# Kernel tuning notes

Hardware: AMD Instinct MI355X
Metric: run time of the kernel (lower is better)

## Reference

```python
import jax, jax.numpy as jnp
import numpy as np

T, B, H, V, D = 128, 16, 8, 25, 64


def setup_inputs() -> dict:
    key = jax.random.key(0)
    k1, k2, k3 = jax.random.split(key, 3)
    q = jax.random.uniform(k1, (T, B, H, V, D), dtype=jnp.float32)
    kv = jax.random.uniform(k2, (T, B, H, V, D), dtype=jnp.float32)
    # decay factor in (0,1), per-head per-channel, as in the torch module
    decay = jax.random.uniform(k3, (1, 1, H, 1, D), dtype=jnp.float32)
    return {"q": q, "kv": kv, "decay": decay}


def reference(q, kv, decay):
    """Decay-based linear recurrent state-space scan (RetNet-style):
        S_t = decay * S_{t-1} + (1 - decay) * kv_t
        out_t = q_t * S_t
    q, kv: (T, B, H, V, D); decay: (1, 1, H, 1, D).
    """
    d = decay[0, 0]          # (H, 1, D), broadcasts against (B, H, V, D)
    one_minus_d = 1.0 - d

    def step(S, qkv_t):
        q_t, kv_t = qkv_t
        S = d * S + one_minus_d * kv_t
        return S, q_t * S

    S0 = jnp.zeros(q.shape[1:], dtype=q.dtype)  # (B, H, V, D)
    _, out = jax.lax.scan(step, S0, (q, kv))
    return out
```

## Files before the change

kernel.cpp:

```cpp
#include <hip/hip_runtime.h>


#define T_DIM 128
#define CH    204800
#define CH4   (CH / 4)
#define VD    (25 * 64)
#define DEPTH 8

typedef float f32x4 __attribute__((ext_vector_type(4)));

__global__ __launch_bounds__(64) void sss_scan_v6(
    const f32x4* __restrict__ q,
    const f32x4* __restrict__ kv,
    const float* __restrict__ decay,
    f32x4* __restrict__ out)
{
    const int i  = blockIdx.x * 64 + threadIdx.x;
    const int e0 = i * 4;
    const int dd = e0 & 63;
    const int h  = (e0 / VD) & 7;

    const f32x4 d   = *(const f32x4*)(decay + h * 64 + dd);
    const f32x4 omd = 1.0f - d;

    const f32x4* __restrict__ qp = q  + i;
    const f32x4* __restrict__ kp = kv + i;
    f32x4*       __restrict__ op = out + i;

    f32x4 S = (f32x4)0.0f;

    f32x4 kbuf[DEPTH], qbuf[DEPTH];

    #pragma unroll
    for (int t = 0; t < DEPTH; ++t) {
        kbuf[t] = kp[(size_t)t * CH4];
        qbuf[t] = qp[(size_t)t * CH4];
    }
    __builtin_amdgcn_sched_barrier(0);

    #pragma unroll
    for (int t = 0; t < T_DIM; ++t) {
        const int j = t & (DEPTH - 1);

        S[0] = fmaf(d[0], S[0], omd[0] * kbuf[j][0]);
        S[1] = fmaf(d[1], S[1], omd[1] * kbuf[j][1]);
        S[2] = fmaf(d[2], S[2], omd[2] * kbuf[j][2]);
        S[3] = fmaf(d[3], S[3], omd[3] * kbuf[j][3]);

        f32x4 o = qbuf[j] * S;
        __builtin_nontemporal_store(o, op + (size_t)t * CH4);

        if (t + DEPTH < T_DIM) {
            kbuf[j] = kp[(size_t)(t + DEPTH) * CH4];
            qbuf[j] = qp[(size_t)(t + DEPTH) * CH4];
        }
        __builtin_amdgcn_sched_barrier(0);
    }
}

extern "C" void kernel_launch(void* const* d_in, const int* in_sizes, int n_in,
                              void* d_out, int out_size, void* d_ws, size_t ws_size,
                              hipStream_t stream) {
    const f32x4* q     = (const f32x4*)d_in[0];
    const f32x4* kv    = (const f32x4*)d_in[1];
    const float* decay = (const float*)d_in[2];
    f32x4* out = (f32x4*)d_out;

    const int threads = 64;
    const int blocks  = CH4 / threads;
    sss_scan_v6<<<blocks, threads, 0, stream>>>(q, kv, decay, out);
}
```

Before: 259.9 us.

## Split time axis across 8 waves with chunked scan and LDS carry combine

Replaces the single-wave sequential scan over all 128 timesteps with a chunked parallel scan: each of 8 waves handles 16 timesteps, computes a local partial state, shares it through LDS, and combines predecessor chunks using decay^16 before a second pass that emits outputs. The aim is more memory-level parallelism and shorter dependency chains per thread. In exchange it does extra FMAs for the second pass, adds a block barrier and LDS traffic, keeps 16 kv vectors in registers, and loses the explicit q prefetch pipeline.

```diff
diff --git a/kernel.cpp b/kernel.cpp
--- a/kernel.cpp
+++ b/kernel.cpp
@@ -5,56 +5,72 @@
 #define CH    204800
 #define CH4   (CH / 4)
 #define VD    (25 * 64)
-#define DEPTH 8
+#define NW    8
+#define LCH   (T_DIM / NW)
 
 typedef float f32x4 __attribute__((ext_vector_type(4)));
 
-__global__ __launch_bounds__(64) void sss_scan_v6(
+__global__ __launch_bounds__(NW * 64) void sss_scan_v7(
     const f32x4* __restrict__ q,
     const f32x4* __restrict__ kv,
     const float* __restrict__ decay,
     f32x4* __restrict__ out)
 {
-    const int i  = blockIdx.x * 64 + threadIdx.x;
-    const int e0 = i * 4;
-    const int dd = e0 & 63;
-    const int h  = (e0 / VD) & 7;
+    __shared__ f32x4 Blds[NW][64];
+
+    const int w    = threadIdx.x >> 6;
+    const int lane = threadIdx.x & 63;
+    const int ci   = blockIdx.x * 64 + lane;
+    const int e0   = ci * 4;
+    const int dd   = e0 & 63;
+    const int h    = (e0 / VD) & 7;
 
     const f32x4 d   = *(const f32x4*)(decay + h * 64 + dd);
     const f32x4 omd = 1.0f - d;
 
-    const f32x4* __restrict__ qp = q  + i;
-    const f32x4* __restrict__ kp = kv + i;
-    f32x4*       __restrict__ op = out + i;
+    const size_t tbase = (size_t)w * LCH;
+    const f32x4* __restrict__ kp = kv  + tbase * CH4 + ci;
+    const f32x4* __restrict__ qp = q   + tbase * CH4 + ci;
+    f32x4*       __restrict__ op = out + tbase * CH4 + ci;
 
+    f32x4 kr[LCH];
+    #pragma unroll
+    for (int j = 0; j < LCH; ++j)
+        kr[j] = kp[(size_t)j * CH4];
+
+    f32x4 B = (f32x4)0.0f;
+    #pragma unroll
+    for (int j = 0; j < LCH; ++j) {
+        B[0] = fmaf(d[0], B[0], omd[0] * kr[j][0]);
+        B[1] = fmaf(d[1], B[1], omd[1] * kr[j][1]);
+        B[2] = fmaf(d[2], B[2], omd[2] * kr[j][2]);
+        B[3] = fmaf(d[3], B[3], omd[3] * kr[j][3]);
+    }
+    Blds[w][lane] = B;
+    __syncthreads();
+
+    f32x4 A = d * d;
+    A = A * A;
+    A = A * A;
+    A = A * A;
     f32x4 S = (f32x4)0.0f;
-
-    f32x4 kbuf[DEPTH], qbuf[DEPTH];
+    for (int wp = 0; wp < w; ++wp) {
+        const f32x4 Bp = Blds[wp][lane];
+        S[0] = fmaf(A[0], S[0], Bp[0]);
+        S[1] = fmaf(A[1], S[1], Bp[1]);
+        S[2] = fmaf(A[2], S[2], Bp[2]);
+        S[3] = fmaf(A[3], S[3], Bp[3]);
+    }
 
     #pragma unroll
-    for (int t = 0; t < DEPTH; ++t) {
-        kbuf[t] = kp[(size_t)t * CH4];
-        qbuf[t] = qp[(size_t)t * CH4];
-    }
-    __builtin_amdgcn_sched_barrier(0);
-
-    #pragma unroll
-    for (int t = 0; t < T_DIM; ++t) {
-        const int j = t & (DEPTH - 1);
-
-        S[0] = fmaf(d[0], S[0], omd[0] * kbuf[j][0]);
-        S[1] = fmaf(d[1], S[1], omd[1] * kbuf[j][1]);
-        S[2] = fmaf(d[2], S[2], omd[2] * kbuf[j][2]);
-        S[3] = fmaf(d[3], S[3], omd[3] * kbuf[j][3]);
-
-        f32x4 o = qbuf[j] * S;
-        __builtin_nontemporal_store(o, op + (size_t)t * CH4);
-
-        if (t + DEPTH < T_DIM) {
-            kbuf[j] = kp[(size_t)(t + DEPTH) * CH4];
-            qbuf[j] = qp[(size_t)(t + DEPTH) * CH4];
-        }
-        __builtin_amdgcn_sched_barrier(0);
+    for (int j = 0; j < LCH; ++j) {
+        const f32x4 qq = qp[(size_t)j * CH4];
+        S[0] = fmaf(d[0], S[0], omd[0] * kr[j][0]);
+        S[1] = fmaf(d[1], S[1], omd[1] * kr[j][1]);
+        S[2] = fmaf(d[2], S[2], omd[2] * kr[j][2]);
+        S[3] = fmaf(d[3], S[3], omd[3] * kr[j][3]);
+        f32x4 o = qq * S;
+        __builtin_nontemporal_store(o, op + (size_t)j * CH4);
     }
 }
 
@@ -66,7 +82,6 @@
     const float* decay = (const float*)d_in[2];
     f32x4* out = (f32x4*)d_out;
 
-    const int threads = 64;
-    const int blocks  = CH4 / threads;
-    sss_scan_v6<<<blocks, threads, 0, stream>>>(q, kv, decay, out);
+    const int blocks = CH4 / 64;
+    sss_scan_v7<<<blocks, NW * 64, 0, stream>>>(q, kv, decay, out);
 }
```

Measured after the change: 263.3 us. About the same (+1.3%).

## Split time axis across waves with chunked scan and LDS carry combine

Applied to the files above, without the earlier changes.

Replaces the per-thread sequential 128-step scan with a two-pass chunked scan. Eight waves per block each handle 16 timesteps and compute a local partial state. The partial states are combined through shared memory with decay^16 weights, and a second pass produces the outputs. Each thread also handles two channel vectors. This exposes more parallelism and memory-level concurrency, at the cost of reading kv twice and dropping the nontemporal stores.

```diff
diff --git a/kernel.cpp b/kernel.cpp
--- a/kernel.cpp
+++ b/kernel.cpp
@@ -2,59 +2,101 @@
 
 
 #define T_DIM 128
-#define CH    204800
-#define CH4   (CH / 4)
-#define VD    (25 * 64)
-#define DEPTH 8
+#define CH4   51200
+#define VD    1600
+#define NW    8
+#define LCH   (T_DIM / NW)
+#define CPT   2
+#define BCH   (64 * CPT)
+#define NBLK  (CH4 / BCH)
 
 typedef float f32x4 __attribute__((ext_vector_type(4)));
 
-__global__ __launch_bounds__(64) void sss_scan_v6(
+__global__ __launch_bounds__(NW * 64, 4) void sss_scan_v8(
     const f32x4* __restrict__ q,
     const f32x4* __restrict__ kv,
     const float* __restrict__ decay,
     f32x4* __restrict__ out)
 {
-    const int i  = blockIdx.x * 64 + threadIdx.x;
-    const int e0 = i * 4;
-    const int dd = e0 & 63;
-    const int h  = (e0 / VD) & 7;
+    __shared__ f32x4 Blds[NW][BCH];
 
-    const f32x4 d   = *(const f32x4*)(decay + h * 64 + dd);
-    const f32x4 omd = 1.0f - d;
+    const int w     = threadIdx.x >> 6;
+    const int lane  = threadIdx.x & 63;
+    const int cbase = blockIdx.x * BCH + lane;
 
-    const f32x4* __restrict__ qp = q  + i;
-    const f32x4* __restrict__ kp = kv + i;
-    f32x4*       __restrict__ op = out + i;
+    f32x4 d2[CPT], omd2[CPT];
+    #pragma unroll
+    for (int c = 0; c < CPT; ++c) {
+        const int ci = cbase + c * 64;
+        const int e0 = ci * 4;
+        const int dd = e0 & 63;
+        const int h  = (e0 / VD) & 7;
+        d2[c]   = *(const f32x4*)(decay + h * 64 + dd);
+        omd2[c] = 1.0f - d2[c];
+    }
 
-    f32x4 S = (f32x4)0.0f;
+    const size_t tb = (size_t)w * LCH;
 
-    f32x4 kbuf[DEPTH], qbuf[DEPTH];
+    f32x4 B[CPT];
+    #pragma unroll
+    for (int c = 0; c < CPT; ++c) B[c] = (f32x4)0.0f;
 
     #pragma unroll
-    for (int t = 0; t < DEPTH; ++t) {
-        kbuf[t] = kp[(size_t)t * CH4];
-        qbuf[t] = qp[(size_t)t * CH4];
+    for (int j = 0; j < LCH; ++j) {
+        f32x4 kk[CPT];
+        #pragma unroll
+        for (int c = 0; c < CPT; ++c)
+            kk[c] = kv[(tb + j) * CH4 + cbase + c * 64];
+        #pragma unroll
+        for (int c = 0; c < CPT; ++c) {
+            B[c][0] = fmaf(d2[c][0], B[c][0], omd2[c][0] * kk[c][0]);
+            B[c][1] = fmaf(d2[c][1], B[c][1], omd2[c][1] * kk[c][1]);
+            B[c][2] = fmaf(d2[c][2], B[c][2], omd2[c][2] * kk[c][2]);
+            B[c][3] = fmaf(d2[c][3], B[c][3], omd2[c][3] * kk[c][3]);
+        }
     }
-    __builtin_amdgcn_sched_barrier(0);
+    #pragma unroll
+    for (int c = 0; c < CPT; ++c)
+        Blds[w][c * 64 + lane] = B[c];
+    __syncthreads();
+
+    f32x4 S[CPT];
+    #pragma unroll
+    for (int c = 0; c < CPT; ++c) {
+        f32x4 A = d2[c] * d2[c];
+        A = A * A;
+        A = A * A;
+        A = A * A;
+        f32x4 s = (f32x4)0.0f;
+        for (int wp = 0; wp < w; ++wp) {
+            const f32x4 Bp = Blds[wp][c * 64 + lane];
+            s[0] = fmaf(A[0], s[0], Bp[0]);
+            s[1] = fmaf(A[1], s[1], Bp[1]);
+            s[2] = fmaf(A[2], s[2], Bp[2]);
+            s[3] = fmaf(A[3], s[3], Bp[3]);
+        }
+        S[c] = s;
+    }
 
     #pragma unroll
-    for (int t = 0; t < T_DIM; ++t) {
-        const int j = t & (DEPTH - 1);
-
-        S[0] = fmaf(d[0], S[0], omd[0] * kbuf[j][0]);
-        S[1] = fmaf(d[1], S[1], omd[1] * kbuf[j][1]);
-        S[2] = fmaf(d[2], S[2], omd[2] * kbuf[j][2]);
-        S[3] = fmaf(d[3], S[3], omd[3] * kbuf[j][3]);
-
-        f32x4 o = qbuf[j] * S;
-        __builtin_nontemporal_store(o, op + (size_t)t * CH4);
-
-        if (t + DEPTH < T_DIM) {
-            kbuf[j] = kp[(size_t)(t + DEPTH) * CH4];
-            qbuf[j] = qp[(size_t)(t + DEPTH) * CH4];
+    for (int j = 0; j < LCH; ++j) {
+        f32x4 kk[CPT], qq[CPT];
+        #pragma unroll
+        for (int c = 0; c < CPT; ++c)
+            kk[c] = kv[(tb + j) * CH4 + cbase + c * 64];
+        #pragma unroll
+        for (int c = 0; c < CPT; ++c)
+            qq[c] = q[(tb + j) * CH4 + cbase + c * 64];
+        #pragma unroll
+        for (int c = 0; c < CPT; ++c) {
+            S[c][0] = fmaf(d2[c][0], S[c][0], omd2[c][0] * kk[c][0]);
+            S[c][1] = fmaf(d2[c][1], S[c][1], omd2[c][1] * kk[c][1]);
+            S[c][2] = fmaf(d2[c][2], S[c][2], omd2[c][2] * kk[c][2]);
+            S[c][3] = fmaf(d2[c][3], S[c][3], omd2[c][3] * kk[c][3]);
+            f32x4 o;
+            o = qq[c] * S[c];
+            out[(tb + j) * CH4 + cbase + c * 64] = o;
         }
-        __builtin_amdgcn_sched_barrier(0);
     }
 }
 
@@ -66,7 +108,5 @@
     const float* decay = (const float*)d_in[2];
     f32x4* out = (f32x4*)d_out;
 
-    const int threads = 64;
-    const int blocks  = CH4 / threads;
-    sss_scan_v6<<<blocks, threads, 0, stream>>>(q, kv, decay, out);
+    sss_scan_v8<<<NBLK, NW * 64, 0, stream>>>(q, kv, decay, out);
 }
```

New measurement: 261.3 us. Within noise of the previous version (+0.5%).
